# Optimization experiments

Hardware: AMD Instinct MI355X
Metric: run time of the kernel (lower is better)

## Reference

```python
import jax, jax.numpy as jnp
import numpy as np

NUM_VIEW = 300
NUM_ANGLE = 12
NUM_DEPTH = 4
GRASP_MAX_WIDTH = 0.1
B, C, NS, NG = 2, 512, 2048, 2000


def generate_grasp_views(N=NUM_VIEW):
    phi = (np.sqrt(5.0) - 1.0) / 2.0  # fibonacci sphere
    idxs = jnp.arange(N, dtype=jnp.float32)
    Z = (2.0 * idxs + 1.0) / N - 1.0
    r = jnp.sqrt(jnp.maximum(1.0 - Z * Z, 0.0))
    X = r * jnp.cos(2.0 * jnp.pi * idxs * phi)
    Y = r * jnp.sin(2.0 * jnp.pi * idxs * phi)
    return jnp.stack([X, Y, Z], -1)  # [N,3]


def viewpoint_params_to_matrix(towards, angle):
    # towards [...,3], angle [...]
    ax = towards
    zero = jnp.zeros_like(ax[..., 0])
    ay = jnp.stack([-ax[..., 1], ax[..., 0], zero], -1)
    ynorm = jnp.linalg.norm(ay, axis=-1, keepdims=True)
    ay = jnp.where(ynorm == 0, jnp.array([0.0, 1.0, 0.0], ax.dtype), ay)
    ax = ax / jnp.linalg.norm(ax, axis=-1, keepdims=True)
    ay = ay / jnp.linalg.norm(ay, axis=-1, keepdims=True)
    az = jnp.cross(ax, ay)
    c, s = jnp.cos(angle), jnp.sin(angle)
    one = jnp.ones_like(c)
    R1 = jnp.stack([one, zero * 0 + jnp.zeros_like(c), jnp.zeros_like(c),
                    jnp.zeros_like(c), c, -s,
                    jnp.zeros_like(c), s, c], -1).reshape(angle.shape + (3, 3))
    R2 = jnp.stack([ax, ay, az], -1)  # axes as columns
    return R2 @ R1


def conv1d(x, w, b):
    # 1x1 Conv1d == channel matmul. x [B,Ci,N], w [Co,Ci]
    return jnp.einsum('oi,bin->bon', w, x) + b[None, :, None]


def knn1(q, ref):
    # K=1 nearest neighbor indices of q [Nq,3] in ref [Nr,3]
    d = (jnp.sum(q * q, -1, keepdims=True) + jnp.sum(ref * ref, -1)[None, :]
         - 2.0 * q @ ref.T)
    return jnp.argmin(d, axis=-1)


def normalize_tensor(t, eps=1e-8):
    mx = jnp.max(t, -1, keepdims=True)
    mn = jnp.min(t, -1, keepdims=True)
    return (t - mn) / (mx - mn + eps)


def _process_one(seed_xyz, pose, gpoints, gscores, gwidths, views, views_rot):
    R, t = pose[:, :3], pose[:, 3]
    gp_trans = gpoints @ R.T + t                      # [Ng,3]
    gv_trans = views @ R.T                            # [V,3]
    gv_rot_trans = jnp.einsum('ij,vjk->vik', R, views_rot)  # [V,3,3]
    view_inds = knn1(views, gv_trans)                 # [V]
    gv_rot_trans = gv_rot_trans[view_inds]            # [V,3,3]
    nn_inds = knn1(seed_xyz, gp_trans)                # [Ns]
    gp_out = gp_trans[nn_inds]                        # [Ns,3]
    # gather seed dim first (Ns<Ng) then reindex views; axes independent
    sc = gscores[nn_inds][:, view_inds]               # [Ns,V,A,D]
    wd = gwidths[nn_inds][:, view_inds]
    rot = jnp.broadcast_to(gv_rot_trans[None], (seed_xyz.shape[0],) + gv_rot_trans.shape)
    return gp_out, rot, sc, wd


def setup_inputs() -> dict:
    key = jax.random.key(0)
    ks = jax.random.split(key, 16)
    seed_features = jax.random.normal(ks[0], (B, C, NS), jnp.float32)
    point_clouds = jax.random.normal(ks[1], (B, NS, 3), jnp.float32) * 0.2
    Rq = np.linalg.qr(np.asarray(jax.random.normal(ks[2], (B, 3, 3))))[0].astype(np.float32)
    trans = jax.random.normal(ks[3], (B, 3, 1), jnp.float32) * 0.1
    object_pose = jnp.concatenate([jnp.asarray(Rq), trans], -1)  # [B,3,4]
    grasp_points = jax.random.normal(ks[4], (B, NG, 3), jnp.float32) * 0.2
    grasp_labels = jax.random.uniform(ks[5], (B, NG, NUM_VIEW, NUM_ANGLE, NUM_DEPTH)) * 1.2 - 0.2
    grasp_offsets = jax.random.uniform(ks[6], (B, NG, NUM_VIEW, NUM_ANGLE, NUM_DEPTH)) * 0.15
    w = lambda k, co, ci: jax.random.normal(k, (co, ci), jnp.float32) * 0.05
    bz = lambda co: jnp.zeros((co,), jnp.float32)
    return {
        'seed_features': seed_features, 'point_clouds': point_clouds,
        'object_pose': object_pose, 'grasp_points': grasp_points,
        'grasp_labels': grasp_labels, 'grasp_offsets': grasp_offsets,
        'aw1_w': w(ks[7], C, C), 'aw1_b': bz(C),
        'aw2_w': w(ks[8], C, C), 'aw2_b': bz(C),
        'aw3_w': w(ks[9], NUM_VIEW, C), 'aw3_b': bz(NUM_VIEW),
        'sw1_w': w(ks[10], C, C), 'sw1_b': bz(C),
        'sw2_w': w(ks[11], NUM_DEPTH * NUM_ANGLE * 2, C), 'sw2_b': bz(NUM_DEPTH * NUM_ANGLE * 2),
    }


def reference(seed_features, point_clouds, object_pose, grasp_points,
              grasp_labels, grasp_offsets, aw1_w, aw1_b, aw2_w, aw2_b,
              aw3_w, aw3_b, sw1_w, sw1_b, sw2_w, sw2_b):
    Bx, Cx, Ns = seed_features.shape
    # --- ApproachNet (eval branch) ---
    res = jax.nn.relu(conv1d(seed_features, aw1_w, aw1_b))
    res = jax.nn.relu(conv1d(res, aw2_w, aw2_b))
    view_scores = conv1d(res, aw3_w, aw3_b).transpose(0, 2, 1)  # [B,Ns,V]
    top_view_inds = jnp.argmax(view_scores, -1)                 # [B,Ns]
    views = generate_grasp_views(NUM_VIEW)
    vp_xyz = views[top_view_inds]                               # [B,Ns,3]
    vp_rot = viewpoint_params_to_matrix(-vp_xyz, jnp.zeros(vp_xyz.shape[:-1], vp_xyz.dtype))
    # --- SWADNet ---
    f = jax.nn.relu(conv1d(res, sw1_w, sw1_b))
    f = conv1d(f, sw2_w, sw2_b)
    f = f.reshape(Bx, 2, NUM_ANGLE, NUM_DEPTH, Ns).transpose(0, 1, 4, 2, 3)
    grasp_score_pred = f[:, 0]   # [B,Ns,A,D]
    grasp_width_pred = f[:, 1]
    # --- process_grasp_labels (vmapped over batch) ---
    views_rot = viewpoint_params_to_matrix(-views, jnp.zeros((NUM_VIEW,), views.dtype))
    gp, rot, sc, wd = jax.vmap(_process_one, in_axes=(0, 0, 0, 0, 0, None, None))(
        point_clouds, object_pose, grasp_points, grasp_labels, grasp_offsets, views, views_rot)
    gmask = (sc <= 0.6) & (sc > 0)
    graspness = normalize_tensor(
        gmask.astype(jnp.float32).reshape(Bx, Ns, NUM_VIEW, -1).mean(-1))  # [B,Ns,V]
    label_mask = (sc > 0) & (wd <= GRASP_MAX_WIDTH)
    sc = jnp.where(label_mask, sc, 0.0)
    # --- match_grasp_view_and_label ---
    bi = jnp.arange(Bx)[:, None]
    ni = jnp.arange(Ns)[None, :]
    top_rot = rot[bi, ni, top_view_inds]  # [B,Ns,3,3]
    top_sc = sc[bi, ni, top_view_inds]    # [B,Ns,A,D]
    top_wd = wd[bi, ni, top_view_inds]
    u_max = jnp.max(top_sc)
    po = top_sc > 0
    safe = jnp.where(po, top_sc, 1.0)
    u_min = jnp.min(jnp.where(po, top_sc, jnp.inf))
    new_sc = jnp.log(u_max / safe) / (jnp.log(u_max / u_min) + 1e-8)
    top_sc = jnp.where(po, new_sc, top_sc)
    return (view_scores, vp_rot, grasp_score_pred, grasp_width_pred,
            top_rot, top_sc, top_wd, graspness, gp)
```

## Files before the change

kernel.cpp:

```cpp
#include <hip/hip_runtime.h>
#include <math.h>

#define NV 300
#define NA 12
#define ND 4
#define NB 2
#define NC 512
#define NSD 2048
#define NGP 2000
#define ROWLEN 14400

__global__ void k_setup(float* __restrict__ views, float* __restrict__ views_rot,
                        int* __restrict__ mmx) {
  int i = threadIdx.x;
  if (i == 0) { mmx[0] = 0; mmx[1] = 0x7f800000; }
  if (i >= NV) return;
  float fi = (float)i;
  float Z = (2.0f * fi + 1.0f) / 300.0f - 1.0f;
  float r = sqrtf(fmaxf(1.0f - Z * Z, 0.0f));
  float ang = (6.28318530717958647692f * fi) * 0.61803398874989484820f;
  float X = r * cosf(ang);
  float Y = r * sinf(ang);
  views[i * 3 + 0] = X; views[i * 3 + 1] = Y; views[i * 3 + 2] = Z;
  float ax0 = -X, ax1 = -Y, ax2 = -Z;
  float ay0 = -ax1, ay1 = ax0, ay2 = 0.f;
  float ynorm = sqrtf(ay0 * ay0 + ay1 * ay1 + ay2 * ay2);
  if (ynorm == 0.f) { ay0 = 0.f; ay1 = 1.f; ay2 = 0.f; }
  float an = sqrtf(ax0 * ax0 + ax1 * ax1 + ax2 * ax2);
  ax0 /= an; ax1 /= an; ax2 /= an;
  float ayn = sqrtf(ay0 * ay0 + ay1 * ay1 + ay2 * ay2);
  ay0 /= ayn; ay1 /= ayn; ay2 /= ayn;
  float az0 = ax1 * ay2 - ax2 * ay1;
  float az1 = ax2 * ay0 - ax0 * ay2;
  float az2 = ax0 * ay1 - ax1 * ay0;
  float* m = views_rot + i * 9;
  m[0] = ax0; m[1] = ay0; m[2] = az0;
  m[3] = ax1; m[4] = ay1; m[5] = az1;
  m[6] = ax2; m[7] = ay2; m[8] = az2;
}

__global__ void __launch_bounds__(512) k_batch_setup(
    const float* __restrict__ pose, const float* __restrict__ views,
    const float* __restrict__ views_rot, int* __restrict__ view_inds,
    float* __restrict__ Rsel) {
  int b = blockIdx.x, tid = threadIdx.x;
  __shared__ float R[9];
  __shared__ float gv[NV][3];
  __shared__ float gvr[NV];
  if (tid < 9) R[tid] = pose[b * 12 + (tid / 3) * 4 + (tid % 3)];
  __syncthreads();
  if (tid < NV) {
    float vx = views[tid * 3], vy = views[tid * 3 + 1], vz = views[tid * 3 + 2];
    float x = R[0] * vx + R[1] * vy + R[2] * vz;
    float y = R[3] * vx + R[4] * vy + R[5] * vz;
    float z = R[6] * vx + R[7] * vy + R[8] * vz;
    gv[tid][0] = x; gv[tid][1] = y; gv[tid][2] = z;
    gvr[tid] = x * x + y * y + z * z;
  }
  __syncthreads();
  if (tid < NV) {
    float qx = views[tid * 3], qy = views[tid * 3 + 1], qz = views[tid * 3 + 2];
    float qq = qx * qx + qy * qy + qz * qz;
    float best = INFINITY; int bi = 0;
    for (int u = 0; u < NV; u++) {
      float dot = qx * gv[u][0] + qy * gv[u][1] + qz * gv[u][2];
      float d = qq + gvr[u] - 2.f * dot;
      if (d < best) { best = d; bi = u; }
    }
    view_inds[b * NV + tid] = bi;
    const float* vr = views_rot + bi * 9;
    float* o = Rsel + (b * NV + tid) * 9;
    for (int i = 0; i < 3; i++)
      for (int j = 0; j < 3; j++)
        o[i * 3 + j] = R[i * 3 + 0] * vr[0 + j] + R[i * 3 + 1] * vr[3 + j] + R[i * 3 + 2] * vr[6 + j];
  }
}

__global__ void k_gp_trans(const float* __restrict__ pose,
                           const float* __restrict__ gpoints,
                           float4* __restrict__ gpt4) {
  int idx = blockIdx.x * 256 + threadIdx.x;
  if (idx >= NB * NGP) return;
  int b = idx / NGP;
  const float* P = pose + b * 12;
  float px = gpoints[(size_t)idx * 3 + 0];
  float py = gpoints[(size_t)idx * 3 + 1];
  float pz = gpoints[(size_t)idx * 3 + 2];
  float x = P[0] * px + P[1] * py + P[2] * pz + P[3];
  float y = P[4] * px + P[5] * py + P[6] * pz + P[7];
  float z = P[8] * px + P[9] * py + P[10] * pz + P[11];
  gpt4[idx] = make_float4(x, y, z, x * x + y * y + z * z);
}

__global__ void __launch_bounds__(256) k_nn(
    const float* __restrict__ pc, const float4* __restrict__ gpt4,
    int* __restrict__ nn_inds, float* __restrict__ out_gp) {
  int b = blockIdx.y;
  int s0 = blockIdx.x * 32;
  int tid = threadIdx.x;
  __shared__ float4 pts[NGP];
  for (int i = tid; i < NGP; i += 256) pts[i] = gpt4[b * NGP + i];
  __syncthreads();
  int sl = tid & 31, chunk = tid >> 5;
  int s = s0 + sl;
  float qx = pc[((size_t)b * NSD + s) * 3 + 0];
  float qy = pc[((size_t)b * NSD + s) * 3 + 1];
  float qz = pc[((size_t)b * NSD + s) * 3 + 2];
  float qq = qx * qx + qy * qy + qz * qz;
  int i0 = chunk * 250;
  float best = INFINITY; int bi = i0;
  for (int i = i0; i < i0 + 250; i++) {
    float4 p = pts[i];
    float d = qq + p.w - 2.f * (qx * p.x + qy * p.y + qz * p.z);
    if (d < best) { best = d; bi = i; }
  }
  __shared__ float rb[8][33];
  __shared__ int ri[8][33];
  rb[chunk][sl] = best; ri[chunk][sl] = bi;
  __syncthreads();
  if (tid < 32) {
    float bb = INFINITY; int ii = 0;
    for (int c = 0; c < 8; c++) {
      float v = rb[c][tid];
      if (v < bb) { bb = v; ii = ri[c][tid]; }
    }
    nn_inds[b * NSD + s0 + tid] = ii;
    float4 p = pts[ii];
    out_gp[((size_t)b * NSD + s0 + tid) * 3 + 0] = p.x;
    out_gp[((size_t)b * NSD + s0 + tid) * 3 + 1] = p.y;
    out_gp[((size_t)b * NSD + s0 + tid) * 3 + 2] = p.z;
  }
}

template <bool RELU, bool GUARD_M>
__global__ void __launch_bounds__(256) gemm128(
    const float* __restrict__ W, const float* __restrict__ X,
    const float* __restrict__ bias, float* __restrict__ Y,
    int O, int Cin, int N) {
  int b = blockIdx.z;
  const float* Xb = X + (size_t)b * Cin * N;
  float* Yb = Y + (size_t)b * O * N;
  int m0 = blockIdx.y * 128, n0 = blockIdx.x * 64;
  __shared__ float As[16][132];
  __shared__ float Bs[16][64];
  int tid = threadIdx.x;
  int mW = tid >> 1;
  int kW = (tid & 1) * 8;
  int kX = tid >> 4, nX = (tid & 15) * 4;
  int ty = tid >> 4, tx = tid & 15;
  bool okm = !GUARD_M || (m0 + mW) < O;
  float4 a0, a1, bv;
  {
    const float* wp = &W[(size_t)(m0 + mW) * Cin + kW];
    a0 = okm ? *(const float4*)wp : make_float4(0.f, 0.f, 0.f, 0.f);
    a1 = okm ? *(const float4*)(wp + 4) : make_float4(0.f, 0.f, 0.f, 0.f);
    bv = *(const float4*)&Xb[(size_t)kX * N + n0 + nX];
  }
  float acc[8][4] = {};
  for (int k0 = 0; k0 < Cin; k0 += 16) {
    __syncthreads();
    As[kW + 0][mW] = a0.x; As[kW + 1][mW] = a0.y;
    As[kW + 2][mW] = a0.z; As[kW + 3][mW] = a0.w;
    As[kW + 4][mW] = a1.x; As[kW + 5][mW] = a1.y;
    As[kW + 6][mW] = a1.z; As[kW + 7][mW] = a1.w;
    *(float4*)&Bs[kX][nX] = bv;
    __syncthreads();
    if (k0 + 16 < Cin) {
      const float* wp = &W[(size_t)(m0 + mW) * Cin + k0 + 16 + kW];
      a0 = okm ? *(const float4*)wp : make_float4(0.f, 0.f, 0.f, 0.f);
      a1 = okm ? *(const float4*)(wp + 4) : make_float4(0.f, 0.f, 0.f, 0.f);
      bv = *(const float4*)&Xb[(size_t)(k0 + 16 + kX) * N + n0 + nX];
    }
#pragma unroll
    for (int kk = 0; kk < 16; kk++) {
      float4 x0 = *(const float4*)&As[kk][ty * 8];
      float4 x1 = *(const float4*)&As[kk][ty * 8 + 4];
      float4 y = *(const float4*)&Bs[kk][tx * 4];
      acc[0][0] = fmaf(x0.x, y.x, acc[0][0]); acc[0][1] = fmaf(x0.x, y.y, acc[0][1]);
      acc[0][2] = fmaf(x0.x, y.z, acc[0][2]); acc[0][3] = fmaf(x0.x, y.w, acc[0][3]);
      acc[1][0] = fmaf(x0.y, y.x, acc[1][0]); acc[1][1] = fmaf(x0.y, y.y, acc[1][1]);
      acc[1][2] = fmaf(x0.y, y.z, acc[1][2]); acc[1][3] = fmaf(x0.y, y.w, acc[1][3]);
      acc[2][0] = fmaf(x0.z, y.x, acc[2][0]); acc[2][1] = fmaf(x0.z, y.y, acc[2][1]);
      acc[2][2] = fmaf(x0.z, y.z, acc[2][2]); acc[2][3] = fmaf(x0.z, y.w, acc[2][3]);
      acc[3][0] = fmaf(x0.w, y.x, acc[3][0]); acc[3][1] = fmaf(x0.w, y.y, acc[3][1]);
      acc[3][2] = fmaf(x0.w, y.z, acc[3][2]); acc[3][3] = fmaf(x0.w, y.w, acc[3][3]);
      acc[4][0] = fmaf(x1.x, y.x, acc[4][0]); acc[4][1] = fmaf(x1.x, y.y, acc[4][1]);
      acc[4][2] = fmaf(x1.x, y.z, acc[4][2]); acc[4][3] = fmaf(x1.x, y.w, acc[4][3]);
      acc[5][0] = fmaf(x1.y, y.x, acc[5][0]); acc[5][1] = fmaf(x1.y, y.y, acc[5][1]);
      acc[5][2] = fmaf(x1.y, y.z, acc[5][2]); acc[5][3] = fmaf(x1.y, y.w, acc[5][3]);
      acc[6][0] = fmaf(x1.z, y.x, acc[6][0]); acc[6][1] = fmaf(x1.z, y.y, acc[6][1]);
      acc[6][2] = fmaf(x1.z, y.z, acc[6][2]); acc[6][3] = fmaf(x1.z, y.w, acc[6][3]);
      acc[7][0] = fmaf(x1.w, y.x, acc[7][0]); acc[7][1] = fmaf(x1.w, y.y, acc[7][1]);
      acc[7][2] = fmaf(x1.w, y.z, acc[7][2]); acc[7][3] = fmaf(x1.w, y.w, acc[7][3]);
    }
  }
#pragma unroll
  for (int i = 0; i < 8; i++) {
    int m = m0 + ty * 8 + i;
    if (GUARD_M && m >= O) break;
    float bi = bias[m];
    float4 v;
    v.x = acc[i][0] + bi; v.y = acc[i][1] + bi;
    v.z = acc[i][2] + bi; v.w = acc[i][3] + bi;
    if (RELU) {
      v.x = fmaxf(v.x, 0.f); v.y = fmaxf(v.y, 0.f);
      v.z = fmaxf(v.z, 0.f); v.w = fmaxf(v.w, 0.f);
    }
    *(float4*)&Yb[(size_t)m * N + n0 + (tx << 2)] = v;
  }
}

template <bool RELU, bool GUARD_M>
__global__ void __launch_bounds__(256) gemm_k(
    const float* __restrict__ W, const float* __restrict__ X,
    const float* __restrict__ bias, float* __restrict__ Y,
    int O, int Cin, int N) {
  int b = blockIdx.z;
  const float* Xb = X + (size_t)b * Cin * N;
  float* Yb = Y + (size_t)b * O * N;
  int m0 = blockIdx.y * 64, n0 = blockIdx.x * 64;
  __shared__ float As[16][68];
  __shared__ float Bs[16][64];
  int tid = threadIdx.x;
  int mW = tid >> 2, kW = (tid & 3) * 4;
  int kX = tid >> 4, nX = (tid & 15) * 4;
  int ty = tid >> 4, tx = tid & 15;
  float acc[4][4] = {};
  for (int k0 = 0; k0 < Cin; k0 += 16) {
    float4 wv;
    if (!GUARD_M || (m0 + mW) < O)
      wv = *(const float4*)&W[(size_t)(m0 + mW) * Cin + k0 + kW];
    else
      wv = make_float4(0.f, 0.f, 0.f, 0.f);
    As[kW + 0][mW] = wv.x; As[kW + 1][mW] = wv.y;
    As[kW + 2][mW] = wv.z; As[kW + 3][mW] = wv.w;
    *(float4*)&Bs[kX][nX] = *(const float4*)&Xb[(size_t)(k0 + kX) * N + n0 + nX];
    __syncthreads();
#pragma unroll
    for (int kk = 0; kk < 16; kk++) {
      float4 a = *(const float4*)&As[kk][ty << 2];
      float4 bv = *(const float4*)&Bs[kk][tx << 2];
      acc[0][0] = fmaf(a.x, bv.x, acc[0][0]); acc[0][1] = fmaf(a.x, bv.y, acc[0][1]);
      acc[0][2] = fmaf(a.x, bv.z, acc[0][2]); acc[0][3] = fmaf(a.x, bv.w, acc[0][3]);
      acc[1][0] = fmaf(a.y, bv.x, acc[1][0]); acc[1][1] = fmaf(a.y, bv.y, acc[1][1]);
      acc[1][2] = fmaf(a.y, bv.z, acc[1][2]); acc[1][3] = fmaf(a.y, bv.w, acc[1][3]);
      acc[2][0] = fmaf(a.z, bv.x, acc[2][0]); acc[2][1] = fmaf(a.z, bv.y, acc[2][1]);
      acc[2][2] = fmaf(a.z, bv.z, acc[2][2]); acc[2][3] = fmaf(a.z, bv.w, acc[2][3]);
      acc[3][0] = fmaf(a.w, bv.x, acc[3][0]); acc[3][1] = fmaf(a.w, bv.y, acc[3][1]);
      acc[3][2] = fmaf(a.w, bv.z, acc[3][2]); acc[3][3] = fmaf(a.w, bv.w, acc[3][3]);
    }
    __syncthreads();
  }
#pragma unroll
  for (int i = 0; i < 4; i++) {
    int m = m0 + ty * 4 + i;
    if (GUARD_M && m >= O) break;
    float bi = bias[m];
    float4 v;
    v.x = acc[i][0] + bi; v.y = acc[i][1] + bi;
    v.z = acc[i][2] + bi; v.w = acc[i][3] + bi;
    if (RELU) {
      v.x = fmaxf(v.x, 0.f); v.y = fmaxf(v.y, 0.f);
      v.z = fmaxf(v.z, 0.f); v.w = fmaxf(v.w, 0.f);
    }
    *(float4*)&Yb[(size_t)m * N + n0 + (tx << 2)] = v;
  }
}

__global__ void __launch_bounds__(256) k_argmax(
    const float* __restrict__ vs_t, const float* __restrict__ views_rot,
    const float* __restrict__ Rsel, int* __restrict__ tv_inds,
    float* __restrict__ o_vprot, float* __restrict__ o_trot) {
  int b = blockIdx.y;
  int s0 = blockIdx.x * 64;
  int tid = threadIdx.x;
  int sl = tid & 63, c = tid >> 6;
  const float* src = vs_t + (size_t)b * NV * NSD + s0 + sl;
  int v0 = c * 75;
  float best = -INFINITY; int bi = v0;
  for (int v = v0; v < v0 + 75; v++) {
    float val = src[(size_t)v * NSD];
    if (val > best) { best = val; bi = v; }
  }
  __shared__ float rb[4][65];
  __shared__ int ri[4][65];
  __shared__ int bia[64];
  rb[c][sl] = best; ri[c][sl] = bi;
  __syncthreads();
  if (tid < 64) {
    float bb = rb[0][tid]; int ii = ri[0][tid];
    for (int cc = 1; cc < 4; cc++) {
      float v = rb[cc][tid];
      if (v > bb) { bb = v; ii = ri[cc][tid]; }
    }
    tv_inds[b * NSD + s0 + tid] = ii;
    bia[tid] = ii;
  }
  __syncthreads();
  for (int idx = tid; idx < 64 * 9; idx += 256) {
    int s2 = idx / 9, j = idx % 9;
    int b2 = bia[s2];
    o_vprot[((size_t)b * NSD + s0 + s2) * 9 + j] = views_rot[b2 * 9 + j];
    o_trot[((size_t)b * NSD + s0 + s2) * 9 + j] = Rsel[(b * NV + b2) * 9 + j];
  }
}

__global__ void k_transpose_vs(const float* __restrict__ vs_t, float* __restrict__ out) {
  __shared__ float tile[32][33];
  int b = blockIdx.z;
  int v0 = blockIdx.x * 32, n0 = blockIdx.y * 32;
  const float* src = vs_t + (size_t)b * NV * NSD;
  for (int i = threadIdx.y; i < 32; i += 8) {
    int v = v0 + i;
    if (v < NV) tile[i][threadIdx.x] = src[(size_t)v * NSD + n0 + threadIdx.x];
  }
  __syncthreads();
  for (int i = threadIdx.y; i < 32; i += 8) {
    int n = n0 + i;
    int v = v0 + threadIdx.x;
    if (v < NV) out[((size_t)b * NSD + n) * NV + v] = tile[threadIdx.x][i];
  }
}

__global__ void __launch_bounds__(256) k_f2(const float* __restrict__ f2,
                                            float* __restrict__ gsp,
                                            float* __restrict__ gwp) {
  __shared__ float tile[96][65];
  int b = blockIdx.y, n0 = blockIdx.x * 64;
  const float* src = f2 + (size_t)b * 96 * NSD;
  for (int idx = threadIdx.x; idx < 96 * 64; idx += 256) {
    int ch = idx >> 6, j = idx & 63;
    tile[ch][j] = src[(size_t)ch * NSD + n0 + j];
  }
  __syncthreads();
  for (int idx = threadIdx.x; idx < 64 * 48; idx += 256) {
    int j = idx / 48, ad = idx % 48;
    size_t o = ((size_t)b * NSD + n0 + j) * 48 + ad;
    gsp[o] = tile[ad][j];
    gwp[o] = tile[48 + ad][j];
  }
}

__global__ void __launch_bounds__(256) k_grasp(
    const float* __restrict__ gscores, const float* __restrict__ goffsets,
    const int* __restrict__ nn_inds, const int* __restrict__ tv_inds,
    const int* __restrict__ view_inds, float* __restrict__ o_grsp,
    float* __restrict__ o_twd, float* __restrict__ raw) {
  __shared__ float row[ROWLEN];
  __shared__ int vi[NV];
  __shared__ float g[NV];
  __shared__ float wmx[4], wmn[4];
  int b = blockIdx.y, s = blockIdx.x, tid = threadIdx.x;
  int nn = nn_inds[b * NSD + s];
  int tv = tv_inds[b * NSD + s];
  for (int v = tid; v < NV; v += 256) vi[v] = view_inds[b * NV + v];
  const float4* src4 = (const float4*)(gscores + (size_t)(b * NGP + nn) * ROWLEN);
  float4* row4 = (float4*)row;
  for (int i = tid; i < ROWLEN / 4; i += 256) row4[i] = src4[i];
  __syncthreads();
  int vit = vi[tv];
  if (tid < 48) {
    float sc = row[vit * 48 + tid];
    float wd = goffsets[(size_t)(b * NGP + nn) * ROWLEN + vit * 48 + tid];
    bool m = (sc > 0.f) && (wd <= 0.1f);
    o_twd[((size_t)b * NSD + s) * 48 + tid] = wd;
    raw[((size_t)b * NSD + s) * 48 + tid] = m ? sc : 0.f;
  }
  int rot = tid & 7;
  for (int v = tid; v < NV; v += 256) {
    const float4* p = (const float4*)(row + vi[v] * 48);
    int cnt = 0;
#pragma unroll
    for (int q0 = 0; q0 < 12; q0++) {
      int q = q0 + rot; if (q >= 12) q -= 12;
      float4 x = p[q];
      cnt += (x.x > 0.f && x.x <= 0.6f);
      cnt += (x.y > 0.f && x.y <= 0.6f);
      cnt += (x.z > 0.f && x.z <= 0.6f);
      cnt += (x.w > 0.f && x.w <= 0.6f);
    }
    g[v] = (float)cnt / 48.0f;
  }
  __syncthreads();
  float mx = -INFINITY, mn = INFINITY;
  for (int v = tid; v < NV; v += 256) { mx = fmaxf(mx, g[v]); mn = fminf(mn, g[v]); }
  for (int off = 32; off; off >>= 1) {
    mx = fmaxf(mx, __shfl_down(mx, off));
    mn = fminf(mn, __shfl_down(mn, off));
  }
  int wid = tid >> 6, lane = tid & 63;
  if (lane == 0) { wmx[wid] = mx; wmn[wid] = mn; }
  __syncthreads();
  if (tid == 0) {
    mx = fmaxf(fmaxf(wmx[0], wmx[1]), fmaxf(wmx[2], wmx[3]));
    mn = fminf(fminf(wmn[0], wmn[1]), fminf(wmn[2], wmn[3]));
    wmx[0] = mx; wmn[0] = mn;
  }
  __syncthreads();
  mx = wmx[0]; mn = wmn[0];
  float denom = mx - mn + 1e-8f;
  float* og = o_grsp + ((size_t)b * NSD + s) * NV;
  for (int v = tid; v < NV; v += 256) og[v] = (g[v] - mn) / denom;
}

__global__ void __launch_bounds__(256) k_reduce(const float* __restrict__ raw,
                                                int n, int* __restrict__ mmx) {
  float mx = -INFINITY, mn = INFINITY;
  for (int i = blockIdx.x * 256 + threadIdx.x; i < n; i += gridDim.x * 256) {
    float v = raw[i];
    mx = fmaxf(mx, v);
    if (v > 0.f) mn = fminf(mn, v);
  }
  for (int off = 32; off; off >>= 1) {
    mx = fmaxf(mx, __shfl_down(mx, off));
    mn = fminf(mn, __shfl_down(mn, off));
  }
  __shared__ float smx[4], smn[4];
  int wid = threadIdx.x >> 6, lane = threadIdx.x & 63;
  if (lane == 0) { smx[wid] = mx; smn[wid] = mn; }
  __syncthreads();
  if (threadIdx.x == 0) {
    mx = fmaxf(fmaxf(smx[0], smx[1]), fmaxf(smx[2], smx[3]));
    mn = fminf(fminf(smn[0], smn[1]), fminf(smn[2], smn[3]));
    atomicMax(&mmx[0], __float_as_int(mx));
    if (mn != INFINITY) atomicMin(&mmx[1], __float_as_int(mn));
  }
}

__global__ void k_topsc(const float* __restrict__ raw, const int* __restrict__ mmx,
                        float* __restrict__ out, int n) {
  int i = blockIdx.x * 256 + threadIdx.x;
  if (i >= n) return;
  float sc = raw[i];
  float umax = __int_as_float(mmx[0]);
  float umin = __int_as_float(mmx[1]);
  float denom = logf(umax / umin) + 1e-8f;
  float val = logf(umax / sc) / denom;
  out[i] = (sc > 0.f) ? val : sc;
}

extern "C" void kernel_launch(void* const* d_in, const int* in_sizes, int n_in,
                              void* d_out, int out_size, void* d_ws, size_t ws_size,
                              hipStream_t stream) {
  const float* seed_features = (const float*)d_in[0];
  const float* point_clouds  = (const float*)d_in[1];
  const float* object_pose   = (const float*)d_in[2];
  const float* grasp_points  = (const float*)d_in[3];
  const float* grasp_labels  = (const float*)d_in[4];
  const float* grasp_offsets = (const float*)d_in[5];
  const float* aw1_w = (const float*)d_in[6];
  const float* aw1_b = (const float*)d_in[7];
  const float* aw2_w = (const float*)d_in[8];
  const float* aw2_b = (const float*)d_in[9];
  const float* aw3_w = (const float*)d_in[10];
  const float* aw3_b = (const float*)d_in[11];
  const float* sw1_w = (const float*)d_in[12];
  const float* sw1_b = (const float*)d_in[13];
  const float* sw2_w = (const float*)d_in[14];
  const float* sw2_b = (const float*)d_in[15];

  float* out = (float*)d_out;
  float* o_vs    = out;
  float* o_vprot = o_vs + NB * NSD * NV;
  float* o_gsp   = o_vprot + NB * NSD * 9;
  float* o_gwp   = o_gsp + NB * NSD * 48;
  float* o_trot  = o_gwp + NB * NSD * 48;
  float* o_tsc   = o_trot + NB * NSD * 9;
  float* o_twd   = o_tsc + NB * NSD * 48;
  float* o_grsp  = o_twd + NB * NSD * 48;
  float* o_gp    = o_grsp + NB * NSD * NV;

  float* w = (float*)d_ws;
  float* res1 = w; w += NB * NC * NSD;
  float* res2 = w; w += NB * NC * NSD;
  float* vs_t = w; w += NB * NV * NSD;
  float* f2   = w; w += NB * 96 * NSD;
  float* views = w; w += 960;
  float* views_rot = w; w += 2720;
  float4* gpt4 = (float4*)w; w += NB * NGP * 4;
  float* Rsel = w; w += NB * NV * 9;
  float* raw  = w; w += NB * NSD * 48;
  int* view_inds = (int*)w; w += NB * NV;
  int* nn_inds   = (int*)w; w += NB * NSD;
  int* tv_inds   = (int*)w; w += NB * NSD;
  int* mmx       = (int*)w; w += 8;

  k_setup<<<1, 512, 0, stream>>>(views, views_rot, mmx);
  k_batch_setup<<<NB, 512, 0, stream>>>(object_pose, views, views_rot, view_inds, Rsel);
  k_gp_trans<<<(NB * NGP + 255) / 256, 256, 0, stream>>>(object_pose, grasp_points, gpt4);
  k_nn<<<dim3(NSD / 32, NB), 256, 0, stream>>>(point_clouds, gpt4, nn_inds, o_gp);

  gemm128<true, false><<<dim3(NSD / 64, NC / 128, NB), 256, 0, stream>>>(
      aw1_w, seed_features, aw1_b, res1, NC, NC, NSD);
  gemm128<true, false><<<dim3(NSD / 64, NC / 128, NB), 256, 0, stream>>>(
      aw2_w, res1, aw2_b, res2, NC, NC, NSD);
  gemm128<false, true><<<dim3(NSD / 64, (NV + 127) / 128, NB), 256, 0, stream>>>(
      aw3_w, res2, aw3_b, vs_t, NV, NC, NSD);
  gemm128<true, false><<<dim3(NSD / 64, NC / 128, NB), 256, 0, stream>>>(
      sw1_w, res2, sw1_b, res1, NC, NC, NSD);
  gemm_k<false, true><<<dim3(NSD / 64, 2, NB), 256, 0, stream>>>(
      sw2_w, res1, sw2_b, f2, 96, NC, NSD);

  k_argmax<<<dim3(NSD / 64, NB), 256, 0, stream>>>(vs_t, views_rot, Rsel, tv_inds,
                                                   o_vprot, o_trot);
  k_transpose_vs<<<dim3((NV + 31) / 32, NSD / 32, NB), dim3(32, 8), 0, stream>>>(vs_t, o_vs);
  k_f2<<<dim3(NSD / 64, NB), 256, 0, stream>>>(f2, o_gsp, o_gwp);
  k_grasp<<<dim3(NSD, NB), 256, 0, stream>>>(grasp_labels, grasp_offsets, nn_inds,
                                             tv_inds, view_inds, o_grsp, o_twd, raw);
  k_reduce<<<256, 256, 0, stream>>>(raw, NB * NSD * 48, mmx);
  k_topsc<<<(NB * NSD * 48 + 255) / 256, 256, 0, stream>>>(raw, mmx, o_tsc, NB * NSD * 48);
}
```

Measured before the change: 707.4 us.

## Precompute per-grasp-point view counts once and double-buffer GEMM shared tiles

The graspness count per view is now computed once per grasp point (NB*NGP rows) in a new k_cnt kernel, not once per seed, and the seed kernel gathers the precomputed counts. This avoids re-reading full 14400-float rows per seed, where 4096 seeds map to only 4000 rows, and also drops the 57KB shared row buffer, which should raise occupancy. The GEMM also gets double-buffered shared tiles, so one barrier per k-step is enough. The cost is an extra workspace buffer, shared-memory atomics in k_cnt, and a full pass over all grasp_labels rows, including rows no seed uses.

Measured after the change: 675.1 us. 1.05x faster.

```diff
diff --git a/kernel.cpp b/kernel.cpp
--- a/kernel.cpp
+++ b/kernel.cpp
@@ -141,8 +141,8 @@
   const float* Xb = X + (size_t)b * Cin * N;
   float* Yb = Y + (size_t)b * O * N;
   int m0 = blockIdx.y * 128, n0 = blockIdx.x * 64;
-  __shared__ float As[16][132];
-  __shared__ float Bs[16][64];
+  __shared__ float As[2][16][132];
+  __shared__ float Bs[2][16][64];
   int tid = threadIdx.x;
   int mW = tid >> 1;
   int kW = (tid & 1) * 8;
@@ -157,25 +157,27 @@
     bv = *(const float4*)&Xb[(size_t)kX * N + n0 + nX];
   }
   float acc[8][4] = {};
-  for (int k0 = 0; k0 < Cin; k0 += 16) {
-    __syncthreads();
-    As[kW + 0][mW] = a0.x; As[kW + 1][mW] = a0.y;
-    As[kW + 2][mW] = a0.z; As[kW + 3][mW] = a0.w;
-    As[kW + 4][mW] = a1.x; As[kW + 5][mW] = a1.y;
-    As[kW + 6][mW] = a1.z; As[kW + 7][mW] = a1.w;
-    *(float4*)&Bs[kX][nX] = bv;
-    __syncthreads();
-    if (k0 + 16 < Cin) {
-      const float* wp = &W[(size_t)(m0 + mW) * Cin + k0 + 16 + kW];
+  int nk = Cin >> 4;
+  for (int kb = 0; kb < nk; kb++) {
+    int buf = kb & 1;
+    As[buf][kW + 0][mW] = a0.x; As[buf][kW + 1][mW] = a0.y;
+    As[buf][kW + 2][mW] = a0.z; As[buf][kW + 3][mW] = a0.w;
+    As[buf][kW + 4][mW] = a1.x; As[buf][kW + 5][mW] = a1.y;
+    As[buf][kW + 6][mW] = a1.z; As[buf][kW + 7][mW] = a1.w;
+    *(float4*)&Bs[buf][kX][nX] = bv;
+    if (kb + 1 < nk) {
+      int k0 = (kb + 1) << 4;
+      const float* wp = &W[(size_t)(m0 + mW) * Cin + k0 + kW];
       a0 = okm ? *(const float4*)wp : make_float4(0.f, 0.f, 0.f, 0.f);
       a1 = okm ? *(const float4*)(wp + 4) : make_float4(0.f, 0.f, 0.f, 0.f);
-      bv = *(const float4*)&Xb[(size_t)(k0 + 16 + kX) * N + n0 + nX];
-    }
+      bv = *(const float4*)&Xb[(size_t)(k0 + kX) * N + n0 + nX];
+    }
+    __syncthreads();
 #pragma unroll
     for (int kk = 0; kk < 16; kk++) {
-      float4 x0 = *(const float4*)&As[kk][ty * 8];
-      float4 x1 = *(const float4*)&As[kk][ty * 8 + 4];
-      float4 y = *(const float4*)&Bs[kk][tx * 4];
+      float4 x0 = *(const float4*)&As[buf][kk][ty * 8];
+      float4 x1 = *(const float4*)&As[buf][kk][ty * 8 + 4];
+      float4 y = *(const float4*)&Bs[buf][kk][tx * 4];
       acc[0][0] = fmaf(x0.x, y.x, acc[0][0]); acc[0][1] = fmaf(x0.x, y.y, acc[0][1]);
       acc[0][2] = fmaf(x0.x, y.z, acc[0][2]); acc[0][3] = fmaf(x0.x, y.w, acc[0][3]);
       acc[1][0] = fmaf(x0.y, y.x, acc[1][0]); acc[1][1] = fmaf(x0.y, y.y, acc[1][1]);
@@ -341,46 +343,50 @@
   }
 }
 
-__global__ void __launch_bounds__(256) k_grasp(
-    const float* __restrict__ gscores, const float* __restrict__ goffsets,
-    const int* __restrict__ nn_inds, const int* __restrict__ tv_inds,
-    const int* __restrict__ view_inds, float* __restrict__ o_grsp,
-    float* __restrict__ o_twd, float* __restrict__ raw) {
-  __shared__ float row[ROWLEN];
+__global__ void __launch_bounds__(256) k_cnt(const float* __restrict__ gscores,
+                                             float* __restrict__ cnt) {
+  int row = blockIdx.x;
+  const float4* src = (const float4*)(gscores + (size_t)row * ROWLEN);
+  __shared__ int c[NV];
+  int tid = threadIdx.x;
+  for (int v = tid; v < NV; v += 256) c[v] = 0;
+  __syncthreads();
+  for (int i = tid; i < ROWLEN / 4; i += 256) {
+    float4 x = src[i];
+    int cc = (x.x > 0.f && x.x <= 0.6f) + (x.y > 0.f && x.y <= 0.6f)
+           + (x.z > 0.f && x.z <= 0.6f) + (x.w > 0.f && x.w <= 0.6f);
+    atomicAdd(&c[i / 12], cc);
+  }
+  __syncthreads();
+  for (int v = tid; v < NV; v += 256)
+    cnt[(size_t)row * NV + v] = (float)c[v] / 48.0f;
+}
+
+__global__ void __launch_bounds__(256) k_gstats(
+    const float* __restrict__ cnt, const float* __restrict__ gscores,
+    const float* __restrict__ goffsets, const int* __restrict__ nn_inds,
+    const int* __restrict__ tv_inds, const int* __restrict__ view_inds,
+    float* __restrict__ o_grsp, float* __restrict__ o_twd,
+    float* __restrict__ raw) {
+  int b = blockIdx.y, s = blockIdx.x, tid = threadIdx.x;
   __shared__ int vi[NV];
   __shared__ float g[NV];
   __shared__ float wmx[4], wmn[4];
-  int b = blockIdx.y, s = blockIdx.x, tid = threadIdx.x;
   int nn = nn_inds[b * NSD + s];
   int tv = tv_inds[b * NSD + s];
   for (int v = tid; v < NV; v += 256) vi[v] = view_inds[b * NV + v];
-  const float4* src4 = (const float4*)(gscores + (size_t)(b * NGP + nn) * ROWLEN);
-  float4* row4 = (float4*)row;
-  for (int i = tid; i < ROWLEN / 4; i += 256) row4[i] = src4[i];
   __syncthreads();
   int vit = vi[tv];
+  size_t rbase = (size_t)(b * NGP + nn);
   if (tid < 48) {
-    float sc = row[vit * 48 + tid];
-    float wd = goffsets[(size_t)(b * NGP + nn) * ROWLEN + vit * 48 + tid];
+    float sc = gscores[rbase * ROWLEN + vit * 48 + tid];
+    float wd = goffsets[rbase * ROWLEN + vit * 48 + tid];
     bool m = (sc > 0.f) && (wd <= 0.1f);
     o_twd[((size_t)b * NSD + s) * 48 + tid] = wd;
     raw[((size_t)b * NSD + s) * 48 + tid] = m ? sc : 0.f;
   }
-  int rot = tid & 7;
-  for (int v = tid; v < NV; v += 256) {
-    const float4* p = (const float4*)(row + vi[v] * 48);
-    int cnt = 0;
-#pragma unroll
-    for (int q0 = 0; q0 < 12; q0++) {
-      int q = q0 + rot; if (q >= 12) q -= 12;
-      float4 x = p[q];
-      cnt += (x.x > 0.f && x.x <= 0.6f);
-      cnt += (x.y > 0.f && x.y <= 0.6f);
-      cnt += (x.z > 0.f && x.z <= 0.6f);
-      cnt += (x.w > 0.f && x.w <= 0.6f);
-    }
-    g[v] = (float)cnt / 48.0f;
-  }
+  const float* crow = cnt + rbase * NV;
+  for (int v = tid; v < NV; v += 256) g[v] = crow[vi[v]];
   __syncthreads();
   float mx = -INFINITY, mn = INFINITY;
   for (int v = tid; v < NV; v += 256) { mx = fmaxf(mx, g[v]); mn = fminf(mn, g[v]); }
@@ -475,6 +481,7 @@
   float* res2 = w; w += NB * NC * NSD;
   float* vs_t = w; w += NB * NV * NSD;
   float* f2   = w; w += NB * 96 * NSD;
+  float* cnt  = w; w += NB * NGP * NV;
   float* views = w; w += 960;
   float* views_rot = w; w += 2720;
   float4* gpt4 = (float4*)w; w += NB * NGP * 4;
@@ -484,6 +491,8 @@
   int* nn_inds   = (int*)w; w += NB * NSD;
   int* tv_inds   = (int*)w; w += NB * NSD;
   int* mmx       = (int*)w; w += 8;
+
+  k_cnt<<<NB * NGP, 256, 0, stream>>>(grasp_labels, cnt);
 
   k_setup<<<1, 512, 0, stream>>>(views, views_rot, mmx);
   k_batch_setup<<<NB, 512, 0, stream>>>(object_pose, views, views_rot, view_inds, Rsel);
@@ -505,8 +514,9 @@
                                                    o_vprot, o_trot);
   k_transpose_vs<<<dim3((NV + 31) / 32, NSD / 32, NB), dim3(32, 8), 0, stream>>>(vs_t, o_vs);
   k_f2<<<dim3(NSD / 64, NB), 256, 0, stream>>>(f2, o_gsp, o_gwp);
-  k_grasp<<<dim3(NSD, NB), 256, 0, stream>>>(grasp_labels, grasp_offsets, nn_inds,
-                                             tv_inds, view_inds, o_grsp, o_twd, raw);
+  k_gstats<<<dim3(NSD, NB), 256, 0, stream>>>(cnt, grasp_labels, grasp_offsets,
+                                              nn_inds, tv_inds, view_inds,
+                                              o_grsp, o_twd, raw);
   k_reduce<<<256, 256, 0, stream>>>(raw, NB * NSD * 48, mmx);
   k_topsc<<<(NB * NSD * 48 + 255) / 256, 256, 0, stream>>>(raw, mmx, o_tsc, NB * NSD * 48);
 }
```
